# Optimization experiments

Measured on AMD Instinct MI355X. Metric: run time of the kernel, lower is better.

## Reference

```python
import jax, jax.numpy as jnp
import numpy as np

DIM = 32          # d_model == channel dim of the volume
D_STATE = 16
D_CONV = 4
EXPAND = 2
D_INNER = EXPAND * DIM        # 64
DT_RANK = max(1, (DIM + 15) // 16)  # ceil(d_model/16) = 2
LN_EPS = 1e-5


def setup_inputs() -> dict:
    key = jax.random.key(0)
    ks = jax.random.split(key, 12)
    B, Dd, Hh, Ww = 1, 32, 32, 32
    sc = 0.02
    x = jax.random.normal(ks[0], (B, DIM, Dd, Hh, Ww), jnp.float32)
    ln_w = jnp.ones((DIM,), jnp.float32)
    ln_b = jnp.zeros((DIM,), jnp.float32)
    in_proj_w = jax.random.normal(ks[1], (2 * D_INNER, DIM), jnp.float32) * sc
    conv_w = jax.random.normal(ks[2], (D_INNER, 1, D_CONV), jnp.float32) * sc
    conv_b = jnp.zeros((D_INNER,), jnp.float32)
    x_proj_w = jax.random.normal(ks[3], (DT_RANK + 2 * D_STATE, D_INNER), jnp.float32) * sc
    dt_proj_w = jax.random.normal(ks[4], (D_INNER, DT_RANK), jnp.float32) * sc
    dt_proj_b = jax.random.uniform(ks[5], (D_INNER,), jnp.float32, -4.0, -2.0)  # small softplus(dt) at init
    # Mamba S4D-real init: A = -[1..d_state], stored as A_log
    A_log = jnp.log(jnp.broadcast_to(jnp.arange(1, D_STATE + 1, dtype=jnp.float32), (D_INNER, D_STATE)))
    D_param = jnp.ones((D_INNER,), jnp.float32)
    out_proj_w = jax.random.normal(ks[6], (DIM, D_INNER), jnp.float32) * sc
    return {
        "x": x, "ln_w": ln_w, "ln_b": ln_b, "in_proj_w": in_proj_w,
        "conv_w": conv_w, "conv_b": conv_b, "x_proj_w": x_proj_w,
        "dt_proj_w": dt_proj_w, "dt_proj_b": dt_proj_b, "A_log": A_log,
        "D_param": D_param, "out_proj_w": out_proj_w,
    }


def _mamba_layer(x, ln_w, ln_b, in_proj_w, conv_w, conv_b, x_proj_w,
                 dt_proj_w, dt_proj_b, A_log, D_param, out_proj_w):
    B, C, Dd, Hh, Ww = x.shape
    L = Dd * Hh * Ww
    # z-scan flatten: (B, C, D, H, W) -> (B, L, C)
    xf = x.reshape(B, C, L).transpose(0, 2, 1)
    # LayerNorm over channel dim
    mu = jnp.mean(xf, axis=-1, keepdims=True)
    var = jnp.mean(jnp.square(xf - mu), axis=-1, keepdims=True)
    xn = (xf - mu) * jax.lax.rsqrt(var + LN_EPS) * ln_w + ln_b
    # in_proj -> x, z branches
    xz = xn @ in_proj_w.T                      # (B, L, 2*d_inner)
    x_in, z = jnp.split(xz, 2, axis=-1)
    # depthwise causal conv1d over sequence
    xt = x_in.transpose(0, 2, 1)               # (B, d_inner, L)
    xc = jax.lax.conv_general_dilated(
        xt, conv_w, window_strides=(1,), padding=[(D_CONV - 1, 0)],
        feature_group_count=D_INNER)
    xc = jax.nn.silu(xc + conv_b[None, :, None]).transpose(0, 2, 1)  # (B, L, d_inner)
    # input-dependent dt, B, C
    x_dbl = xc @ x_proj_w.T                    # (B, L, dt_rank + 2*d_state)
    dt, Bm, Cm = jnp.split(x_dbl, [DT_RANK, DT_RANK + D_STATE], axis=-1)
    delta = jax.nn.softplus(dt @ dt_proj_w.T + dt_proj_b)            # (B, L, d_inner)
    A = -jnp.exp(A_log)                        # (d_inner, d_state)
    # discretize: h_t = exp(delta*A) h_{t-1} + delta*B_t*x_t
    dA = jnp.exp(delta[..., None] * A)                               # (B, L, d_inner, d_state)
    dBx = delta[..., None] * Bm[:, :, None, :] * xc[..., None]       # (B, L, d_inner, d_state)
    def comb(e1, e2):
        a1, b1 = e1
        a2, b2 = e2
        return (a1 * a2, a2 * b1 + b2)
    _, h = jax.lax.associative_scan(comb, (dA, dBx), axis=1)         # parallel linear recurrence
    y = jnp.einsum('blds,bls->bld', h, Cm) + xc * D_param            # (B, L, d_inner)
    y = y * jax.nn.silu(z)
    out = y @ out_proj_w.T                     # (B, L, C)
    # unpermute z-scan
    return out.transpose(0, 2, 1).reshape(B, C, Dd, Hh, Ww)


def reference(x, ln_w, ln_b, in_proj_w, conv_w, conv_b, x_proj_w,
              dt_proj_w, dt_proj_b, A_log, D_param, out_proj_w):
    return _mamba_layer(x, ln_w, ln_b, in_proj_w, conv_w, conv_b, x_proj_w,
                        dt_proj_w, dt_proj_b, A_log, D_param, out_proj_w)
```

## Files before the change

### kernel.cpp

```cpp
#include <hip/hip_runtime.h>
#include <hip/hip_bf16.h>

constexpr int L   = 32768;
constexpr int CD  = 32;
constexpr int DI  = 64;
constexpr int DS  = 16;
constexpr int LC  = 64;
constexpr int NCH = L / LC;
constexpr int NPAIR = DI * DS;

constexpr size_t FL        = (size_t)DI * L;
constexpr size_t OFF_SZ    = 0;
constexpr size_t OFF_XC    = FL;
constexpr size_t OFF_DELTA = 2 * FL;
constexpr size_t OFF_BM    = 3 * FL;
constexpr size_t OFF_CM    = OFF_BM + (size_t)DS * L;
constexpr size_t OFF_APROD = OFF_CM + (size_t)DS * L;
constexpr size_t OFF_CARRY = OFF_APROD;
constexpr size_t OFF_BACC  = OFF_APROD + (size_t)NCH * NPAIR;

__device__ __forceinline__ float bf2f(__hip_bfloat16 v) { return __bfloat162float(v); }
__device__ __forceinline__ void f4arr(const float4 v, float* a) { a[0]=v.x; a[1]=v.y; a[2]=v.z; a[3]=v.w; }

__device__ __forceinline__ bool detect_bf16(const void* ln_w) {
    return ((const unsigned short*)ln_w)[0] == 0x3F80;
}
__device__ __forceinline__ float ldin(const void* p, size_t i, bool bf16) {
    return bf16 ? bf2f(((const __hip_bfloat16*)p)[i]) : ((const float*)p)[i];
}

__global__ __launch_bounds__(256) void k12_featurize_scan(
    const void* __restrict__ x,
    const void* __restrict__ ln_w,
    const void* __restrict__ ln_b,
    const void* __restrict__ in_proj_w,
    const void* __restrict__ conv_w,
    const void* __restrict__ conv_b,
    const void* __restrict__ x_proj_w,
    const void* __restrict__ dt_proj_w,
    const void* __restrict__ dt_proj_b,
    const void* __restrict__ A_log,
    float* __restrict__ ws)
{
    __shared__ __align__(16) char smem[67840];
    float (*xin_s)[69]  = (float(*)[69])(smem);
    char* AR = smem + 17664;
    float (*xn_s)[33]   = (float(*)[33])(AR);
    float (*w_in_s)[32] = (float(*)[32])(AR + 8848);
    float (*sdl)[68]    = (float(*)[68])(AR);
    float (*sxc)[68]    = (float(*)[68])(AR + 17408);
    float (*sbm)[68]    = (float(*)[68])(AR + 34816);
    char* FW = smem + 56832;
    float (*w_xp)[64]   = (float(*)[64])(FW);
    float (*w_cv)[4]    = (float(*)[4])(FW + 8704);
    float (*w_dt)[2]    = (float(*)[2])(FW + 9728);
    float* b_dt_s = (float*)(FW + 10240);
    float* b_cv_s = (float*)(FW + 10496);
    float* lnw_s  = (float*)(FW + 10752);
    float* lnb_s  = (float*)(FW + 10880);

    const int tid = threadIdx.x;
    const int l0  = blockIdx.x * LC;
    const bool isb = detect_bf16(ln_w);

    if (isb) {
        const __hip_bfloat16* ipw = (const __hip_bfloat16*)in_proj_w;
        const __hip_bfloat16* xpw = (const __hip_bfloat16*)x_proj_w;
        for (int i = tid; i < 128 * 32; i += 256) w_in_s[i >> 5][i & 31] = bf2f(ipw[i]);
        for (int i = tid; i < 34 * 64; i += 256)  w_xp[i >> 6][i & 63] = bf2f(xpw[i]);
    } else {
        const float* ipw = (const float*)in_proj_w;
        const float* xpw = (const float*)x_proj_w;
        for (int i = tid; i < 128 * 32; i += 256) w_in_s[i >> 5][i & 31] = ipw[i];
        for (int i = tid; i < 34 * 64; i += 256)  w_xp[i >> 6][i & 63] = xpw[i];
    }
    w_cv[tid >> 2][tid & 3] = ldin(conv_w, tid, isb);
    if (tid < 128) w_dt[tid >> 1][tid & 1] = ldin(dt_proj_w, tid, isb);
    if (tid < 64) { b_dt_s[tid] = ldin(dt_proj_b, tid, isb); b_cv_s[tid] = ldin(conv_b, tid, isb); }
    if (tid < 32) { lnw_s[tid] = ldin(ln_w, tid, isb); lnb_s[tid] = ldin(ln_b, tid, isb); }
    __syncthreads();

    if (tid < LC + 3) {
        const int l = l0 - 3 + tid;
        const bool valid = (l >= 0);
        const int lc = valid ? l : 0;
        float xv[CD];
        if (isb) {
            const __hip_bfloat16* xb = (const __hip_bfloat16*)x;
            #pragma unroll
            for (int c = 0; c < CD; ++c) xv[c] = bf2f(xb[(size_t)c * L + lc]);
        } else {
            const float* xf = (const float*)x;
            #pragma unroll
            for (int c = 0; c < CD; ++c) xv[c] = xf[(size_t)c * L + lc];
        }
        float mu = 0.f;
        #pragma unroll
        for (int c = 0; c < CD; ++c) mu += xv[c];
        mu *= (1.f / CD);
        float var = 0.f;
        #pragma unroll
        for (int c = 0; c < CD; ++c) { const float dc = xv[c] - mu; var += dc * dc; }
        const float rstd = rsqrtf(var * (1.f / CD) + 1e-5f);
        #pragma unroll
        for (int c = 0; c < CD; ++c)
            xn_s[tid][c] = valid ? ((xv[c] - mu) * rstd * lnw_s[c] + lnb_s[c]) : 0.f;
    }
    __syncthreads();

    {
        const int wv   = tid >> 6;
        const int lane = tid & 63;
        const int jb   = wv * 32;
        if (wv < 2) {
            const int pos1  = 64 + lane;
            const bool v1   = (pos1 < LC + 3);
            const int pos1c = v1 ? pos1 : 66;
            float xv0[CD], xv1[CD];
            #pragma unroll
            for (int c = 0; c < CD; ++c) { xv0[c] = xn_s[lane][c]; xv1[c] = xn_s[pos1c][c]; }
            for (int j = 0; j < 32; ++j) {
                const float4* wr = (const float4*)w_in_s[jb + j];
                float a0 = 0.f, a1 = 0.f;
                #pragma unroll
                for (int q = 0; q < 8; ++q) {
                    const float4 w4 = wr[q];
                    a0 += w4.x * xv0[4*q] + w4.y * xv0[4*q+1] + w4.z * xv0[4*q+2] + w4.w * xv0[4*q+3];
                    a1 += w4.x * xv1[4*q] + w4.y * xv1[4*q+1] + w4.z * xv1[4*q+2] + w4.w * xv1[4*q+3];
                }
                xin_s[jb + j][lane] = a0;
                if (v1) xin_s[jb + j][pos1] = a1;
            }
        } else {
            const int l = l0 + lane;
            float xv[CD];
            #pragma unroll
            for (int c = 0; c < CD; ++c) xv[c] = xn_s[3 + lane][c];
            for (int j = 0; j < 32; ++j) {
                const float4* wr = (const float4*)w_in_s[jb + j];
                float acc = 0.f;
                #pragma unroll
                for (int q = 0; q < 8; ++q) {
                    const float4 w4 = wr[q];
                    acc += w4.x * xv[4*q] + w4.y * xv[4*q+1] + w4.z * xv[4*q+2] + w4.w * xv[4*q+3];
                }
                const float s = acc / (1.f + __expf(-acc));
                ws[OFF_SZ + (size_t)(jb - 64 + j) * L + l] = s;
            }
        }
    }
    __syncthreads();

    {
        const int h  = tid & 3;
        const int pq = tid >> 2;
        const int l  = l0 + pq;
        const int dbase = h * 16;
        float xcv[16];
        #pragma unroll
        for (int i = 0; i < 16; ++i) {
            const int d = dbase + i;
            float acc = b_cv_s[d];
            #pragma unroll
            for (int k = 0; k < 4; ++k) acc += w_cv[d][k] * xin_s[d][pq + k];
            const float v = acc / (1.f + __expf(-acc));
            xcv[i] = v;
            ws[OFF_XC + (size_t)d * L + l] = v;
            sxc[d][pq] = v;
        }
        float dt0 = 0.f, dt1 = 0.f;
        for (int r = 0; r < 34; ++r) {
            float acc = 0.f;
            #pragma unroll
            for (int i = 0; i < 16; ++i) acc += w_xp[r][dbase + i] * xcv[i];
            acc += __shfl_xor(acc, 1);
            acc += __shfl_xor(acc, 2);
            if (r == 0) dt0 = acc;
            else if (r == 1) dt1 = acc;
            else {
                const int rr = r - 2;
                if (h == (rr >> 3)) {
                    const size_t off = (rr < 16) ? (OFF_BM + (size_t)rr * L)
                                                 : (OFF_CM + (size_t)(rr - 16) * L);
                    ws[off + l] = acc;
                    if (rr < 16) sbm[rr][pq] = acc;
                }
            }
        }
        #pragma unroll
        for (int i = 0; i < 16; ++i) {
            const int d = dbase + i;
            const float tv = dt0 * w_dt[d][0] + dt1 * w_dt[d][1] + b_dt_s[d];
            const float sp = fmaxf(tv, 0.f) + log1pf(__expf(-fabsf(tv)));
            ws[OFF_DELTA + (size_t)d * L + l] = sp;
            sdl[d][pq] = sp;
        }
    }
    __syncthreads();

    {
        const int d = tid >> 2, sg = tid & 3;
        float Aj[4], ap[4] = {1.f, 1.f, 1.f, 1.f}, bb[4] = {0.f, 0.f, 0.f, 0.f};
        #pragma unroll
        for (int j = 0; j < 4; ++j) Aj[j] = -__expf(ldin(A_log, d * DS + sg + 4 * j, isb));

        for (int t = 0; t < LC; t += 4) {
            float ddv[4], xxv[4], bm[4][4];
            f4arr(*(const float4*)&sdl[d][t], ddv);
            f4arr(*(const float4*)&sxc[d][t], xxv);
            f4arr(*(const float4*)&sbm[sg][t],      bm[0]);
            f4arr(*(const float4*)&sbm[sg + 4][t],  bm[1]);
            f4arr(*(const float4*)&sbm[sg + 8][t],  bm[2]);
            f4arr(*(const float4*)&sbm[sg + 12][t], bm[3]);
            #pragma unroll
            for (int tt = 0; tt < 4; ++tt) {
                const float dxc = ddv[tt] * xxv[tt];
                #pragma unroll
                for (int j = 0; j < 4; ++j) {
                    const float e = __expf(ddv[tt] * Aj[j]);
                    ap[j] *= e;
                    bb[j] = e * bb[j] + dxc * bm[j][tt];
                }
            }
        }
        #pragma unroll
        for (int j = 0; j < 4; ++j) {
            const size_t p = (size_t)(tid * 4 + j);
            ws[OFF_APROD + p * NCH + blockIdx.x] = ap[j];
            ws[OFF_BACC  + p * NCH + blockIdx.x] = bb[j];
        }
    }
}

__global__ __launch_bounds__(256) void k3_carry(float* __restrict__ ws)
{
    const int lane = threadIdx.x & 63;
    const int p    = blockIdx.x * 4 + (threadIdx.x >> 6);
    const size_t row_a = OFF_APROD + (size_t)p * NCH;
    const size_t row_b = OFF_BACC  + (size_t)p * NCH;

    float a[8], b[8];
    f4arr(*(const float4*)&ws[row_a + lane * 8],     a);
    f4arr(*(const float4*)&ws[row_a + lane * 8 + 4], a + 4);
    f4arr(*(const float4*)&ws[row_b + lane * 8],     b);
    f4arr(*(const float4*)&ws[row_b + lane * 8 + 4], b + 4);

    float Ag = a[0], Bg = b[0];
    #pragma unroll
    for (int i = 1; i < 8; ++i) { Bg = a[i] * Bg + b[i]; Ag = Ag * a[i]; }
    #pragma unroll
    for (int off = 1; off < 64; off <<= 1) {
        const float pa = __shfl_up(Ag, off);
        const float pb = __shfl_up(Bg, off);
        if (lane >= off) { Bg = Ag * pb + Bg; Ag = Ag * pa; }
    }
    float Pb = __shfl_up(Bg, 1);
    if (lane == 0) Pb = 0.f;
    float cr[8];
    #pragma unroll
    for (int i = 0; i < 8; ++i) { cr[i] = Pb; Pb = a[i] * Pb + b[i]; }
    *(float4*)&ws[OFF_CARRY + (size_t)p * NCH + lane * 8]     = make_float4(cr[0], cr[1], cr[2], cr[3]);
    *(float4*)&ws[OFF_CARRY + (size_t)p * NCH + lane * 8 + 4] = make_float4(cr[4], cr[5], cr[6], cr[7]);
}

__global__ __launch_bounds__(256, 3) void k45_apply_out(
    const void* __restrict__ A_log,
    const void* __restrict__ D_param,
    const void* __restrict__ ln_w,
    const void* __restrict__ out_proj_w,
    float* __restrict__ ws,
    void* __restrict__ out)
{
    __shared__ __align__(16) float sbm[DS][68];
    __shared__ __align__(16) float scm[DS][68];
    __shared__ __align__(16) float sy[DI][68];
    __shared__ float w_out_s[CD][DI];
    const int tid = threadIdx.x;
    const int c   = blockIdx.x;
    const size_t t0 = (size_t)c * LC;
    const bool isb = detect_bf16(ln_w);

    if (isb) {
        const __hip_bfloat16* opw = (const __hip_bfloat16*)out_proj_w;
        for (int i = tid; i < CD * DI; i += 256) w_out_s[i >> 6][i & 63] = bf2f(opw[i]);
    } else {
        const float* opw = (const float*)out_proj_w;
        for (int i = tid; i < CD * DI; i += 256) w_out_s[i >> 6][i & 63] = opw[i];
    }
    {
        const int r = tid >> 4, t4 = (tid & 15) * 4;
        *(float4*)&sbm[r][t4] = *(const float4*)&ws[OFF_BM + (size_t)r * L + t0 + t4];
        *(float4*)&scm[r][t4] = *(const float4*)&ws[OFF_CM + (size_t)r * L + t0 + t4];
    }

    const int d = tid >> 2, sg = tid & 3;
    float Aj[4];
    #pragma unroll
    for (int j = 0; j < 4; ++j) Aj[j] = -__expf(ldin(A_log, d * DS + sg + 4 * j, isb));
    const float Dd = ldin(D_param, d, isb);
    float hh[4];
    #pragma unroll
    for (int j = 0; j < 4; ++j) hh[j] = ws[OFF_CARRY + (size_t)(tid * 4 + j) * NCH + c];
    __syncthreads();

    const float* dlp = ws + OFF_DELTA + (size_t)d * L + t0;
    const float* xcp = ws + OFF_XC    + (size_t)d * L + t0;
    float4 dd4 = *(const float4*)dlp;
    float4 xx4 = *(const float4*)xcp;
    for (int t = 0; t < LC; t += 4) {
        const int tn = (t + 4) & 63;
        const float4 ddn = *(const float4*)(dlp + tn);
        const float4 xxn = *(const float4*)(xcp + tn);
        float ddv[4], xxv[4], bm[4][4], cm[4][4];
        f4arr(dd4, ddv);
        f4arr(xx4, xxv);
        f4arr(*(const float4*)&sbm[sg][t],      bm[0]);
        f4arr(*(const float4*)&sbm[sg + 4][t],  bm[1]);
        f4arr(*(const float4*)&sbm[sg + 8][t],  bm[2]);
        f4arr(*(const float4*)&sbm[sg + 12][t], bm[3]);
        f4arr(*(const float4*)&scm[sg][t],      cm[0]);
        f4arr(*(const float4*)&scm[sg + 4][t],  cm[1]);
        f4arr(*(const float4*)&scm[sg + 8][t],  cm[2]);
        f4arr(*(const float4*)&scm[sg + 12][t], cm[3]);
        #pragma unroll
        for (int tt = 0; tt < 4; ++tt) {
            const float dxc = ddv[tt] * xxv[tt];
            float ys = 0.f;
            #pragma unroll
            for (int j = 0; j < 4; ++j) {
                const float e = __expf(ddv[tt] * Aj[j]);
                hh[j] = e * hh[j] + dxc * bm[j][tt];
                ys += hh[j] * cm[j][tt];
            }
            ys += __shfl_xor(ys, 1);
            ys += __shfl_xor(ys, 2);
            if (sg == 0) sy[d][t + tt] = ys + xxv[tt] * Dd;
        }
        dd4 = ddn; xx4 = xxn;
    }
    __syncthreads();

    #pragma unroll
    for (int k = 0; k < 4; ++k) {
        const int idx = tid + k * 256;
        const int r = idx >> 4, t4 = (idx & 15) * 4;
        float4 yv = *(float4*)&sy[r][t4];
        const float4 zv = *(const float4*)&ws[OFF_SZ + (size_t)r * L + t0 + t4];
        yv.x *= zv.x; yv.y *= zv.y; yv.z *= zv.z; yv.w *= zv.w;
        *(float4*)&sy[r][t4] = yv;
    }
    __syncthreads();

    {
        const int wv   = tid >> 6;
        const int lane = tid & 63;
        float acc[8] = {0.f, 0.f, 0.f, 0.f, 0.f, 0.f, 0.f, 0.f};
        for (int dd = 0; dd < DI; ++dd) {
            const float yv = sy[dd][lane];
            #pragma unroll
            for (int j = 0; j < 8; ++j)
                acc[j] += yv * w_out_s[wv * 8 + j][dd];
        }
        const size_t l = t0 + lane;
        #pragma unroll
        for (int j = 0; j < 8; ++j) {
            const int cc = wv * 8 + j;
            if (isb) ((__hip_bfloat16*)out)[(size_t)cc * L + l] = __float2bfloat16(acc[j]);
            else     ((float*)out)[(size_t)cc * L + l] = acc[j];
        }
    }
}

extern "C" void kernel_launch(void* const* d_in, const int* in_sizes, int n_in,
                              void* d_out, int out_size, void* d_ws, size_t ws_size,
                              hipStream_t stream)
{
    (void)in_sizes; (void)n_in; (void)out_size; (void)ws_size;
    const void* x        = d_in[0];
    const void* ln_w     = d_in[1];
    const void* ln_b     = d_in[2];
    const void* in_pw    = d_in[3];
    const void* conv_w   = d_in[4];
    const void* conv_b   = d_in[5];
    const void* x_pw     = d_in[6];
    const void* dt_pw    = d_in[7];
    const void* dt_pb    = d_in[8];
    const void* A_log    = d_in[9];
    const void* D_param  = d_in[10];
    const void* out_pw   = d_in[11];
    float* ws = (float*)d_ws;

    k12_featurize_scan<<<NCH, 256, 0, stream>>>(x, ln_w, ln_b, in_pw, conv_w, conv_b,
                                                x_pw, dt_pw, dt_pb, A_log, ws);
    k3_carry<<<NPAIR / 4, 256, 0, stream>>>(ws);
    k45_apply_out<<<NCH, 256, 0, stream>>>(A_log, D_param, ln_w, out_pw, ws, d_out);
}
```

Baseline: 160.6 us.

## Halve apply-chunk length, store z/xc intermediates in bf16, transpose chunk summaries

The first kernel now emits chunk summaries for 32-step half-chunks, stored pair-contiguous so the writes are float4. The carry kernel scans 1024 summaries per pair with strided loads. The apply/out kernel runs over twice as many blocks with 32-step chunks, which shortens each block's serial scan and raises parallelism. The gate and conv-output intermediates are written and read as bf16 to cut workspace traffic, at some cost in precision and uncoalesced reads in the carry kernel.

Measured after the change: 207.7 us. 29.3% more time.

```diff
diff --git a/kernel.cpp b/kernel.cpp
--- a/kernel.cpp
+++ b/kernel.cpp
@@ -7,19 +7,21 @@
 constexpr int DS  = 16;
 constexpr int LC  = 64;
 constexpr int NCH = L / LC;
+constexpr int LH  = 32;
+constexpr int NHC = L / LH;
 constexpr int NPAIR = DI * DS;
 
-constexpr size_t FL        = (size_t)DI * L;
 constexpr size_t OFF_SZ    = 0;
-constexpr size_t OFF_XC    = FL;
-constexpr size_t OFF_DELTA = 2 * FL;
-constexpr size_t OFF_BM    = 3 * FL;
-constexpr size_t OFF_CM    = OFF_BM + (size_t)DS * L;
-constexpr size_t OFF_APROD = OFF_CM + (size_t)DS * L;
-constexpr size_t OFF_CARRY = OFF_APROD;
-constexpr size_t OFF_BACC  = OFF_APROD + (size_t)NCH * NPAIR;
+constexpr size_t OFF_XC    = 1048576;
+constexpr size_t OFF_DELTA = 2097152;
+constexpr size_t OFF_BM    = 4194304;
+constexpr size_t OFF_CM    = 4718592;
+constexpr size_t OFF_APROD = 5242880;
+constexpr size_t OFF_BACC  = 6291456;
+constexpr size_t OFF_CT    = 7340032;
 
 __device__ __forceinline__ float bf2f(__hip_bfloat16 v) { return __bfloat162float(v); }
+__device__ __forceinline__ float bfu(unsigned short u) { return __uint_as_float(((unsigned)u) << 16); }
 __device__ __forceinline__ void f4arr(const float4 v, float* a) { a[0]=v.x; a[1]=v.y; a[2]=v.z; a[3]=v.w; }
 
 __device__ __forceinline__ bool detect_bf16(const void* ln_w) {
@@ -62,6 +64,8 @@
     const int tid = threadIdx.x;
     const int l0  = blockIdx.x * LC;
     const bool isb = detect_bf16(ln_w);
+    __hip_bfloat16* sz_bf = (__hip_bfloat16*)(ws + OFF_SZ);
+    __hip_bfloat16* xc_bf = (__hip_bfloat16*)(ws + OFF_XC);
 
     if (isb) {
         const __hip_bfloat16* ipw = (const __hip_bfloat16*)in_proj_w;
@@ -145,7 +149,7 @@
                     acc += w4.x * xv[4*q] + w4.y * xv[4*q+1] + w4.z * xv[4*q+2] + w4.w * xv[4*q+3];
                 }
                 const float s = acc / (1.f + __expf(-acc));
-                ws[OFF_SZ + (size_t)(jb - 64 + j) * L + l] = s;
+                sz_bf[(size_t)(jb - 64 + j) * L + l] = __float2bfloat16(s);
             }
         }
     }
@@ -165,7 +169,7 @@
             for (int k = 0; k < 4; ++k) acc += w_cv[d][k] * xin_s[d][pq + k];
             const float v = acc / (1.f + __expf(-acc));
             xcv[i] = v;
-            ws[OFF_XC + (size_t)d * L + l] = v;
+            xc_bf[(size_t)d * L + l] = __float2bfloat16(v);
             sxc[d][pq] = v;
         }
         float dt0 = 0.f, dt1 = 0.f;
@@ -200,34 +204,35 @@
 
     {
         const int d = tid >> 2, sg = tid & 3;
-        float Aj[4], ap[4] = {1.f, 1.f, 1.f, 1.f}, bb[4] = {0.f, 0.f, 0.f, 0.f};
+        float Aj[4];
         #pragma unroll
         for (int j = 0; j < 4; ++j) Aj[j] = -__expf(ldin(A_log, d * DS + sg + 4 * j, isb));
 
-        for (int t = 0; t < LC; t += 4) {
-            float ddv[4], xxv[4], bm[4][4];
-            f4arr(*(const float4*)&sdl[d][t], ddv);
-            f4arr(*(const float4*)&sxc[d][t], xxv);
-            f4arr(*(const float4*)&sbm[sg][t],      bm[0]);
-            f4arr(*(const float4*)&sbm[sg + 4][t],  bm[1]);
-            f4arr(*(const float4*)&sbm[sg + 8][t],  bm[2]);
-            f4arr(*(const float4*)&sbm[sg + 12][t], bm[3]);
-            #pragma unroll
-            for (int tt = 0; tt < 4; ++tt) {
-                const float dxc = ddv[tt] * xxv[tt];
+        #pragma unroll
+        for (int half = 0; half < 2; ++half) {
+            float ap[4] = {1.f, 1.f, 1.f, 1.f}, bb[4] = {0.f, 0.f, 0.f, 0.f};
+            for (int t = half * 32; t < half * 32 + 32; t += 4) {
+                float ddv[4], xxv[4], bm[4][4];
+                f4arr(*(const float4*)&sdl[d][t], ddv);
+                f4arr(*(const float4*)&sxc[d][t], xxv);
+                f4arr(*(const float4*)&sbm[sg][t],      bm[0]);
+                f4arr(*(const float4*)&sbm[sg + 4][t],  bm[1]);
+                f4arr(*(const float4*)&sbm[sg + 8][t],  bm[2]);
+                f4arr(*(const float4*)&sbm[sg + 12][t], bm[3]);
                 #pragma unroll
-                for (int j = 0; j < 4; ++j) {
-                    const float e = __expf(ddv[tt] * Aj[j]);
-                    ap[j] *= e;
-                    bb[j] = e * bb[j] + dxc * bm[j][tt];
+                for (int tt = 0; tt < 4; ++tt) {
+                    const float dxc = ddv[tt] * xxv[tt];
+                    #pragma unroll
+                    for (int j = 0; j < 4; ++j) {
+                        const float e = __expf(ddv[tt] * Aj[j]);
+                        ap[j] *= e;
+                        bb[j] = e * bb[j] + dxc * bm[j][tt];
+                    }
                 }
             }
-        }
-        #pragma unroll
-        for (int j = 0; j < 4; ++j) {
-            const size_t p = (size_t)(tid * 4 + j);
-            ws[OFF_APROD + p * NCH + blockIdx.x] = ap[j];
-            ws[OFF_BACC  + p * NCH + blockIdx.x] = bb[j];
+            const size_t o = (size_t)(2 * blockIdx.x + half) * NPAIR + tid * 4;
+            *(float4*)&ws[OFF_APROD + o] = make_float4(ap[0], ap[1], ap[2], ap[3]);
+            *(float4*)&ws[OFF_BACC + o]  = make_float4(bb[0], bb[1], bb[2], bb[3]);
         }
     }
 }
@@ -236,18 +241,17 @@
 {
     const int lane = threadIdx.x & 63;
     const int p    = blockIdx.x * 4 + (threadIdx.x >> 6);
-    const size_t row_a = OFF_APROD + (size_t)p * NCH;
-    const size_t row_b = OFF_BACC  + (size_t)p * NCH;
-
-    float a[8], b[8];
-    f4arr(*(const float4*)&ws[row_a + lane * 8],     a);
-    f4arr(*(const float4*)&ws[row_a + lane * 8 + 4], a + 4);
-    f4arr(*(const float4*)&ws[row_b + lane * 8],     b);
-    f4arr(*(const float4*)&ws[row_b + lane * 8 + 4], b + 4);
-
+
+    float a[16], b[16];
+    #pragma unroll
+    for (int i = 0; i < 16; ++i) {
+        const size_t c = (size_t)(lane * 16 + i);
+        a[i] = ws[OFF_APROD + c * NPAIR + p];
+        b[i] = ws[OFF_BACC  + c * NPAIR + p];
+    }
     float Ag = a[0], Bg = b[0];
     #pragma unroll
-    for (int i = 1; i < 8; ++i) { Bg = a[i] * Bg + b[i]; Ag = Ag * a[i]; }
+    for (int i = 1; i < 16; ++i) { Bg = a[i] * Bg + b[i]; Ag = Ag * a[i]; }
     #pragma unroll
     for (int off = 1; off < 64; off <<= 1) {
         const float pa = __shfl_up(Ag, off);
@@ -256,14 +260,16 @@
     }
     float Pb = __shfl_up(Bg, 1);
     if (lane == 0) Pb = 0.f;
-    float cr[8];
-    #pragma unroll
-    for (int i = 0; i < 8; ++i) { cr[i] = Pb; Pb = a[i] * Pb + b[i]; }
-    *(float4*)&ws[OFF_CARRY + (size_t)p * NCH + lane * 8]     = make_float4(cr[0], cr[1], cr[2], cr[3]);
-    *(float4*)&ws[OFF_CARRY + (size_t)p * NCH + lane * 8 + 4] = make_float4(cr[4], cr[5], cr[6], cr[7]);
-}
-
-__global__ __launch_bounds__(256, 3) void k45_apply_out(
+    float cr[16];
+    #pragma unroll
+    for (int i = 0; i < 16; ++i) { cr[i] = Pb; Pb = a[i] * Pb + b[i]; }
+    const size_t rb = OFF_CT + (size_t)p * NHC + lane * 16;
+    #pragma unroll
+    for (int k = 0; k < 4; ++k)
+        *(float4*)&ws[rb + 4 * k] = make_float4(cr[4*k], cr[4*k+1], cr[4*k+2], cr[4*k+3]);
+}
+
+__global__ __launch_bounds__(256, 4) void k45_apply_out(
     const void* __restrict__ A_log,
     const void* __restrict__ D_param,
     const void* __restrict__ ln_w,
@@ -271,14 +277,16 @@
     float* __restrict__ ws,
     void* __restrict__ out)
 {
-    __shared__ __align__(16) float sbm[DS][68];
-    __shared__ __align__(16) float scm[DS][68];
-    __shared__ __align__(16) float sy[DI][68];
+    __shared__ __align__(16) float sbm[DS][36];
+    __shared__ __align__(16) float scm[DS][36];
+    __shared__ __align__(16) float sy[DI][36];
     __shared__ float w_out_s[CD][DI];
     const int tid = threadIdx.x;
-    const int c   = blockIdx.x;
-    const size_t t0 = (size_t)c * LC;
+    const int hb  = blockIdx.x;
+    const size_t t0 = (size_t)hb * LH;
     const bool isb = detect_bf16(ln_w);
+    const __hip_bfloat16* sz_bf = (const __hip_bfloat16*)(ws + OFF_SZ);
+    const __hip_bfloat16* xc_bf = (const __hip_bfloat16*)(ws + OFF_XC);
 
     if (isb) {
         const __hip_bfloat16* opw = (const __hip_bfloat16*)out_proj_w;
@@ -288,9 +296,9 @@
         for (int i = tid; i < CD * DI; i += 256) w_out_s[i >> 6][i & 63] = opw[i];
     }
     {
-        const int r = tid >> 4, t4 = (tid & 15) * 4;
-        *(float4*)&sbm[r][t4] = *(const float4*)&ws[OFF_BM + (size_t)r * L + t0 + t4];
-        *(float4*)&scm[r][t4] = *(const float4*)&ws[OFF_CM + (size_t)r * L + t0 + t4];
+        const int q = tid & 7, r = (tid >> 3) & 15;
+        if (tid < 128) *(float4*)&sbm[r][q * 4] = *(const float4*)&ws[OFF_BM + (size_t)r * L + t0 + q * 4];
+        else           *(float4*)&scm[r][q * 4] = *(const float4*)&ws[OFF_CM + (size_t)r * L + t0 + q * 4];
     }
 
     const int d = tid >> 2, sg = tid & 3;
@@ -300,20 +308,20 @@
     const float Dd = ldin(D_param, d, isb);
     float hh[4];
     #pragma unroll
-    for (int j = 0; j < 4; ++j) hh[j] = ws[OFF_CARRY + (size_t)(tid * 4 + j) * NCH + c];
+    for (int j = 0; j < 4; ++j) hh[j] = ws[OFF_CT + (size_t)(tid * 4 + j) * NHC + hb];
     __syncthreads();
 
     const float* dlp = ws + OFF_DELTA + (size_t)d * L + t0;
-    const float* xcp = ws + OFF_XC    + (size_t)d * L + t0;
+    const __hip_bfloat16* xcp = xc_bf + (size_t)d * L + t0;
     float4 dd4 = *(const float4*)dlp;
-    float4 xx4 = *(const float4*)xcp;
-    for (int t = 0; t < LC; t += 4) {
-        const int tn = (t + 4) & 63;
+    ushort4 xu4 = *(const ushort4*)xcp;
+    for (int t = 0; t < LH; t += 4) {
+        const int tn = (t + 4) & (LH - 1);
         const float4 ddn = *(const float4*)(dlp + tn);
-        const float4 xxn = *(const float4*)(xcp + tn);
+        const ushort4 xun = *(const ushort4*)(xcp + tn);
         float ddv[4], xxv[4], bm[4][4], cm[4][4];
         f4arr(dd4, ddv);
-        f4arr(xx4, xxv);
+        xxv[0] = bfu(xu4.x); xxv[1] = bfu(xu4.y); xxv[2] = bfu(xu4.z); xxv[3] = bfu(xu4.w);
         f4arr(*(const float4*)&sbm[sg][t],      bm[0]);
         f4arr(*(const float4*)&sbm[sg + 4][t],  bm[1]);
         f4arr(*(const float4*)&sbm[sg + 8][t],  bm[2]);
@@ -336,35 +344,35 @@
             ys += __shfl_xor(ys, 2);
             if (sg == 0) sy[d][t + tt] = ys + xxv[tt] * Dd;
         }
-        dd4 = ddn; xx4 = xxn;
-    }
-    __syncthreads();
-
-    #pragma unroll
-    for (int k = 0; k < 4; ++k) {
+        dd4 = ddn; xu4 = xun;
+    }
+    __syncthreads();
+
+    #pragma unroll
+    for (int k = 0; k < 2; ++k) {
         const int idx = tid + k * 256;
-        const int r = idx >> 4, t4 = (idx & 15) * 4;
+        const int r = idx >> 3, t4 = (idx & 7) * 4;
         float4 yv = *(float4*)&sy[r][t4];
-        const float4 zv = *(const float4*)&ws[OFF_SZ + (size_t)r * L + t0 + t4];
-        yv.x *= zv.x; yv.y *= zv.y; yv.z *= zv.z; yv.w *= zv.w;
+        const ushort4 zu = *(const ushort4*)(sz_bf + (size_t)r * L + t0 + t4);
+        yv.x *= bfu(zu.x); yv.y *= bfu(zu.y); yv.z *= bfu(zu.z); yv.w *= bfu(zu.w);
         *(float4*)&sy[r][t4] = yv;
     }
     __syncthreads();
 
     {
-        const int wv   = tid >> 6;
-        const int lane = tid & 63;
-        float acc[8] = {0.f, 0.f, 0.f, 0.f, 0.f, 0.f, 0.f, 0.f};
+        const int g   = tid >> 5;
+        const int pos = tid & 31;
+        float acc[4] = {0.f, 0.f, 0.f, 0.f};
         for (int dd = 0; dd < DI; ++dd) {
-            const float yv = sy[dd][lane];
-            #pragma unroll
-            for (int j = 0; j < 8; ++j)
-                acc[j] += yv * w_out_s[wv * 8 + j][dd];
-        }
-        const size_t l = t0 + lane;
-        #pragma unroll
-        for (int j = 0; j < 8; ++j) {
-            const int cc = wv * 8 + j;
+            const float yv = sy[dd][pos];
+            #pragma unroll
+            for (int j = 0; j < 4; ++j)
+                acc[j] += yv * w_out_s[g * 4 + j][dd];
+        }
+        const size_t l = t0 + pos;
+        #pragma unroll
+        for (int j = 0; j < 4; ++j) {
+            const int cc = g * 4 + j;
             if (isb) ((__hip_bfloat16*)out)[(size_t)cc * L + l] = __float2bfloat16(acc[j]);
             else     ((float*)out)[(size_t)cc * L + l] = acc[j];
         }
@@ -393,5 +401,5 @@
     k12_featurize_scan<<<NCH, 256, 0, stream>>>(x, ln_w, ln_b, in_pw, conv_w, conv_b,
                                                 x_pw, dt_pw, dt_pb, A_log, ws);
     k3_carry<<<NPAIR / 4, 256, 0, stream>>>(ws);
-    k45_apply_out<<<NCH, 256, 0, stream>>>(A_log, D_param, ln_w, out_pw, ws, d_out);
-}
+    k45_apply_out<<<NHC, 256, 0, stream>>>(A_log, D_param, ln_w, out_pw, ws, d_out);
+}
```
